# Performance work log

Measured on AMD Instinct MI355X. Metric: run time of the kernel, lower is better.

## Reference

```python
import jax, jax.numpy as jnp
import numpy as np

N, D, K, H = 16384, 2048, 8, 8
HD = D // H
LN_EPS = 1e-5


def setup_inputs() -> dict:
    key = jax.random.key(0)
    ks = jax.random.split(key, 12)
    w = lambda k: jax.random.normal(k, (D, D), dtype=jnp.float32) * 0.02
    return {
        "hidden": jax.random.normal(ks[0], (N, D), dtype=jnp.float32),
        "memory": jax.random.normal(ks[1], (K, D), dtype=jnp.float32) * 0.02,
        "w_read_q": w(ks[2]), "w_read_k": w(ks[3]), "w_read_v": w(ks[4]),
        "w_read_out": w(ks[5]),
        "w_write_q": w(ks[6]), "w_write_k": w(ks[7]), "w_write_v": w(ks[8]),
        "ln_gamma": jnp.ones((D,), dtype=jnp.float32),
        "ln_beta": jnp.zeros((D,), dtype=jnp.float32),
        "gate": jnp.full((1,), -3.0, dtype=jnp.float32),
        "write_gate": jnp.full((1,), -2.0, dtype=jnp.float32),
    }


def _layernorm(x, gamma, beta):
    mu = jnp.mean(x, axis=-1, keepdims=True)
    var = jnp.mean(jnp.square(x - mu), axis=-1, keepdims=True)
    return (x - mu) * jax.lax.rsqrt(var + LN_EPS) * gamma + beta


def reference(hidden, memory, w_read_q, w_read_k, w_read_v, w_read_out,
              w_write_q, w_write_k, w_write_v, ln_gamma, ln_beta, gate, write_gate):
    # --- read: cross-attention from tokens (queries) to memory slots (keys/values) ---
    q = (hidden @ w_read_q.T).reshape(N, H, HD)   # [N,H,hd]
    k = (memory @ w_read_k.T).reshape(K, H, HD)   # [K,H,hd]
    v = (memory @ w_read_v.T).reshape(K, H, HD)
    scores = jnp.einsum("nhd,khd->hnk", q, k) / np.sqrt(HD).astype(np.float32)
    attn = jax.nn.softmax(scores, axis=-1)        # [H,N,K]
    read_out = jnp.einsum("hnk,khd->nhd", attn, v).reshape(N, D)
    cross_info = _layernorm(read_out, ln_gamma, ln_beta) @ w_read_out.T
    g = jax.nn.sigmoid(gate[0])
    result = hidden + g * cross_info              # [N,D]
    # --- write: memory slots (queries) attend over all tokens, gated EMA update ---
    wq = memory @ w_write_q.T                     # [K,D]
    wk = hidden @ w_write_k.T                     # [N,D]
    wv = hidden @ w_write_v.T                     # [N,D]
    wattn = jax.nn.softmax(wq @ wk.T / np.sqrt(D).astype(np.float32), axis=-1)  # [K,N]
    new_info = wattn @ wv                         # [K,D]
    wg = jax.nn.sigmoid(write_gate[0])
    new_memory = (1.0 - wg) * memory + wg * new_info
    return result, new_memory
```

## Files before the change

kernel.cpp:

```cpp
#include <hip/hip_runtime.h>
#include <hip/hip_bf16.h>
#include <stdint.h>

static constexpr int N_ = 16384;
static constexpr int D_ = 2048;
static constexpr float SCALE_R = 1.0f / 16.0f;
static constexpr float SCALE_W = 0.02209708691207961f;

typedef __bf16 bf16x8 __attribute__((ext_vector_type(8)));
typedef float f32x4 __attribute__((ext_vector_type(4)));

__device__ __forceinline__ unsigned short f2bf(float f) {
  unsigned int u = __float_as_uint(f);
  unsigned int r = (u + 0x7fff + ((u >> 16) & 1)) >> 16;
  return (unsigned short)r;
}

__device__ __forceinline__ void lds_load16(void* lds, const void* g) {
  __builtin_amdgcn_global_load_lds(
      (const __attribute__((address_space(1))) uint32_t*)(uintptr_t)g,
      (__attribute__((address_space(3))) uint32_t*)(uint32_t)(uintptr_t)lds,
      16, 0, 0);
}

__global__ __launch_bounds__(256) void k_kvwq(
    const float* __restrict__ mem, const float* __restrict__ wrk,
    const float* __restrict__ wrv, const float* __restrict__ wwq,
    float* __restrict__ kbuf, float* __restrict__ vbuf, float* __restrict__ wqbuf) {
  int gw = (blockIdx.x * 256 + threadIdx.x) >> 6;
  int lane = threadIdx.x & 63;
  int which = gw >> 11;
  int j = gw & 2047;
  const float* W = which == 0 ? wrk : (which == 1 ? wrv : wwq);
  float* O = which == 0 ? kbuf : (which == 1 ? vbuf : wqbuf);
  const f32x4* Wrow = (const f32x4*)(W + (size_t)j * D_);
  const f32x4* M4 = (const f32x4*)mem;
  float acc[8];
#pragma unroll
  for (int kk = 0; kk < 8; ++kk) acc[kk] = 0.f;
#pragma unroll
  for (int t = 0; t < 8; ++t) {
    f32x4 w4 = Wrow[lane + 64 * t];
#pragma unroll
    for (int kk = 0; kk < 8; ++kk) {
      f32x4 m4 = M4[kk * 512 + lane + 64 * t];
      acc[kk] += w4[0] * m4[0] + w4[1] * m4[1] + w4[2] * m4[2] + w4[3] * m4[3];
    }
  }
#pragma unroll
  for (int off = 1; off < 64; off <<= 1)
#pragma unroll
    for (int kk = 0; kk < 8; ++kk) acc[kk] += __shfl_xor(acc[kk], off, 64);
  if (lane == 0) {
#pragma unroll
    for (int kk = 0; kk < 8; ++kk) O[kk * D_ + j] = acc[kk];
  }
}

__global__ __launch_bounds__(256) void k_pr(
    const float* __restrict__ wrq, const float* __restrict__ wwk,
    const float* __restrict__ kbuf, const float* __restrict__ wqbuf,
    float* __restrict__ PRT) {
  int b = blockIdx.x;
  int tid = threadIdx.x;
  bool isP = b < 256;
  int bb = isP ? b : b - 256;
  int q = bb & 3;
  int sub = (bb >> 2) & 7;
  int ic = bb >> 5;
  int i = ic * 256 + tid;
  const float* W = isP ? wrq : wwk;
  const float* V = isP ? kbuf : wqbuf;
  float scale = isP ? SCALE_R : SCALE_W;
  int rowbase = isP ? sub * 8 : 64;
  float acc[8];
#pragma unroll
  for (int kk = 0; kk < 8; ++kk) acc[kk] = 0.f;
  int j0 = sub * 256 + q * 64;
#pragma unroll 4
  for (int jj = 0; jj < 64; ++jj) {
    int j = j0 + jj;
    float wv = W[(size_t)j * D_ + i];
#pragma unroll
    for (int kk = 0; kk < 8; ++kk) acc[kk] += wv * V[kk * D_ + j];
  }
#pragma unroll
  for (int kk = 0; kk < 8; ++kk)
    atomicAdd(&PRT[(rowbase + kk) * D_ + i], acc[kk] * scale);
}

__global__ __launch_bounds__(256) void k_prtb(const float* __restrict__ PRT,
                                              unsigned short* __restrict__ PRTb) {
  int i = (blockIdx.x * 256 + threadIdx.x) * 4;
  f32x4 v = *(const f32x4*)(PRT + i);
  ushort4 o = {f2bf(v[0]), f2bf(v[1]), f2bf(v[2]), f2bf(v[3])};
  *(ushort4*)(PRTb + i) = o;
}

__global__ __launch_bounds__(256) void k_prep(const float* __restrict__ wro,
                                              const float* __restrict__ gamma,
                                              const float* __restrict__ beta,
                                              unsigned short* __restrict__ wp,
                                              float* __restrict__ c1, float* __restrict__ c2) {
  __shared__ float red1[4], red2[4];
  int j = blockIdx.x;
  int tid = threadIdx.x;
  int d = tid * 8;
  const float* src = wro + (size_t)j * D_ + d;
  f32x4 a = *(const f32x4*)src, b = *(const f32x4*)(src + 4);
  f32x4 g0 = *(const f32x4*)(gamma + d), g1 = *(const f32x4*)(gamma + d + 4);
  f32x4 b0 = *(const f32x4*)(beta + d), b1 = *(const f32x4*)(beta + d + 4);
  ushort4 o0, o1;
  o0.x = f2bf(a[0] * g0[0]); o0.y = f2bf(a[1] * g0[1]);
  o0.z = f2bf(a[2] * g0[2]); o0.w = f2bf(a[3] * g0[3]);
  o1.x = f2bf(b[0] * g1[0]); o1.y = f2bf(b[1] * g1[1]);
  o1.z = f2bf(b[2] * g1[2]); o1.w = f2bf(b[3] * g1[3]);
  unsigned short* dst = wp + (size_t)j * D_ + d;
  *(ushort4*)dst = o0;
  *(ushort4*)(dst + 4) = o1;
  float s1 = a[0] * g0[0] + a[1] * g0[1] + a[2] * g0[2] + a[3] * g0[3] +
             b[0] * g1[0] + b[1] * g1[1] + b[2] * g1[2] + b[3] * g1[3];
  float s2 = a[0] * b0[0] + a[1] * b0[1] + a[2] * b0[2] + a[3] * b0[3] +
             b[0] * b1[0] + b[1] * b1[1] + b[2] * b1[2] + b[3] * b1[3];
#pragma unroll
  for (int off = 1; off < 64; off <<= 1) {
    s1 += __shfl_xor(s1, off, 64);
    s2 += __shfl_xor(s2, off, 64);
  }
  int wave = tid >> 6, lane = tid & 63;
  if (lane == 0) { red1[wave] = s1; red2[wave] = s2; }
  __syncthreads();
  if (tid == 0) {
    c1[j] = red1[0] + red1[1] + red1[2] + red1[3];
    c2[j] = red2[0] + red2[1] + red2[2] + red2[3];
  }
}

__global__ __launch_bounds__(256) void k_main(
    const float* __restrict__ hidden, const unsigned short* __restrict__ PRTb,
    const float* __restrict__ vbuf,
    unsigned short* __restrict__ Xhat, float* __restrict__ mu_out,
    float* __restrict__ rstd_out,
    float* __restrict__ upart, float* __restrict__ Zpart) {
  __shared__ unsigned short Ah[2][64 * 64];
  __shared__ unsigned short Bh[2][80 * 64];
  __shared__ unsigned short attnL[64 * 64];
  __shared__ float e8lds[64][8];
  const int tid = threadIdx.x;
  const int row0 = blockIdx.x * 64;
  const int wave = tid >> 6, lane = tid & 63;
  const int fl = lane & 15, fk = lane >> 4;
  const int ar = tid >> 2, acg = tid & 3;

  f32x4 sA0[4], sA1[4];

  auto loadA = [&](f32x4* a, int t) {
    const float* srcA = hidden + (size_t)(row0 + ar) * D_ + t * 64 + acg * 16;
#pragma unroll
    for (int q = 0; q < 4; ++q) a[q] = *(const f32x4*)(srcA + q * 4);
  };
  auto writeA = [&](int buf, f32x4* a) {
#pragma unroll
    for (int hh = 0; hh < 2; ++hh) {
      f32x4 x = a[hh * 2], y = a[hh * 2 + 1];
      ushort4 o0 = {f2bf(x[0]), f2bf(x[1]), f2bf(x[2]), f2bf(x[3])};
      ushort4 o1 = {f2bf(y[0]), f2bf(y[1]), f2bf(y[2]), f2bf(y[3])};
      int idx = (ar * 64 + acg * 16 + hh * 8) ^ ((ar & 7) << 3);
      *(ushort4*)&Ah[buf][idx] = o0;
      *(ushort4*)&Ah[buf][idx + 4] = o1;
    }
  };
  auto stageB = [&](int buf, int kt) {
#pragma unroll
    for (int s = 0; s < 2; ++s) {
      int e = s * 256 + tid;
      int rB = e >> 3, gl = e & 7, gs = gl ^ (rB & 7);
      lds_load16(&Bh[buf][rB * 64 + gl * 8],
                 PRTb + (size_t)rB * D_ + kt * 64 + gs * 8);
    }
    if (tid < 128) {
      int e = 512 + tid;
      int rB = e >> 3, gl = e & 7, gs = gl ^ (rB & 7);
      lds_load16(&Bh[buf][rB * 64 + gl * 8],
                 PRTb + (size_t)rB * D_ + kt * 64 + gs * 8);
    }
  };

  f32x4 acc[5];
#pragma unroll
  for (int n = 0; n < 5; ++n) acc[n] = (f32x4){0.f, 0.f, 0.f, 0.f};

  auto compute = [&](int buf) {
#pragma unroll
    for (int kk = 0; kk < 2; ++kk) {
      int klo = kk * 32 + fk * 8;
      bf16x8 af = *(const bf16x8*)&Ah[buf][((wave * 16 + fl) * 64 + klo) ^ ((fl & 7) << 3)];
#pragma unroll
      for (int n = 0; n < 5; ++n) {
        bf16x8 bf = *(const bf16x8*)&Bh[buf][((n * 16 + fl) * 64 + klo) ^ ((fl & 7) << 3)];
        acc[n] = __builtin_amdgcn_mfma_f32_16x16x32_bf16(af, bf, acc[n], 0, 0, 0);
      }
    }
  };

  loadA(sA0, 0);
  loadA(sA1, 1);
  stageB(0, 0);
  for (int t = 0; t < 32; t += 2) {
    writeA(0, sA0);
    if (t + 2 < 32) loadA(sA0, t + 2);
    __syncthreads();
    stageB(1, t + 1);
    compute(0);
    writeA(1, sA1);
    if (t + 3 < 32) loadA(sA1, t + 3);
    __syncthreads();
    if (t + 2 < 32) stageB(0, t + 2);
    compute(1);
  }

#pragma unroll
  for (int r = 0; r < 4; ++r) {
    int rowl = wave * 16 + fk * 4 + r;
#pragma unroll
    for (int n = 0; n < 4; ++n) {
      float sv = acc[n][r];
      float m = sv;
      m = fmaxf(m, __shfl_xor(m, 1, 64));
      m = fmaxf(m, __shfl_xor(m, 2, 64));
      m = fmaxf(m, __shfl_xor(m, 4, 64));
      float e = __expf(sv - m);
      float ssum = e;
      ssum += __shfl_xor(ssum, 1, 64);
      ssum += __shfl_xor(ssum, 2, 64);
      ssum += __shfl_xor(ssum, 4, 64);
      attnL[rowl * 64 + n * 16 + fl] = f2bf(e / ssum);
    }
    if (fl < 8) e8lds[rowl][fl] = __expf(acc[4][r]);
  }
  __syncthreads();

  float ssum[16], ssq[16];
#pragma unroll
  for (int rw = 0; rw < 16; ++rw) { ssum[rw] = 0.f; ssq[rw] = 0.f; }
#pragma unroll
  for (int c = 0; c < 8; ++c) {
    int d0 = c * 256 + lane * 4;
    f32x4 vv[8];
#pragma unroll
    for (int kk = 0; kk < 8; ++kk) vv[kk] = *(const f32x4*)(vbuf + kk * D_ + d0);
#pragma unroll
    for (int rw = 0; rw < 16; ++rw) {
      bf16x8 at = *(const bf16x8*)&attnL[(wave * 16 + rw) * 64 + c * 8];
      f32x4 ro = (float)at[0] * vv[0] + (float)at[1] * vv[1] +
                 (float)at[2] * vv[2] + (float)at[3] * vv[3] +
                 (float)at[4] * vv[4] + (float)at[5] * vv[5] +
                 (float)at[6] * vv[6] + (float)at[7] * vv[7];
      ssum[rw] += ro[0] + ro[1] + ro[2] + ro[3];
      ssq[rw] += ro[0] * ro[0] + ro[1] * ro[1] + ro[2] * ro[2] + ro[3] * ro[3];
      ushort4 o = {f2bf(ro[0]), f2bf(ro[1]), f2bf(ro[2]), f2bf(ro[3])};
      *(ushort4*)(Xhat + (size_t)(row0 + wave * 16 + rw) * D_ + d0) = o;
    }
  }
  float muv = 0.f, rstdv = 0.f;
#pragma unroll
  for (int rw = 0; rw < 16; ++rw) {
    float s = ssum[rw], q = ssq[rw];
#pragma unroll
    for (int off = 1; off < 64; off <<= 1) {
      s += __shfl_xor(s, off, 64);
      q += __shfl_xor(q, off, 64);
    }
    float m = s * (1.f / 2048.f);
    float var = q * (1.f / 2048.f) - m * m;
    float rs = rsqrtf(var + 1e-5f);
    if (lane == rw) { muv = m; rstdv = rs; }
  }
  if (lane < 16) {
    mu_out[row0 + wave * 16 + lane] = muv;
    rstd_out[row0 + wave * 16 + lane] = rstdv;
  }
  __syncthreads();

  for (int dt = 0; dt < 2; ++dt) {
    int d0 = wave * 512 + dt * 256 + lane * 4;
    f32x4 ua[8];
#pragma unroll
    for (int kk = 0; kk < 8; ++kk) ua[kk] = (f32x4){0.f, 0.f, 0.f, 0.f};
    for (int r8 = 0; r8 < 64; r8 += 8) {
      f32x4 hv[8];
#pragma unroll
      for (int q = 0; q < 8; ++q)
        hv[q] = *(const f32x4*)(hidden + (size_t)(row0 + r8 + q) * D_ + d0);
#pragma unroll
      for (int q = 0; q < 8; ++q) {
        f32x4 e0 = *(const f32x4*)&e8lds[r8 + q][0];
        f32x4 e1 = *(const f32x4*)&e8lds[r8 + q][4];
        ua[0] += e0[0] * hv[q]; ua[1] += e0[1] * hv[q];
        ua[2] += e0[2] * hv[q]; ua[3] += e0[3] * hv[q];
        ua[4] += e1[0] * hv[q]; ua[5] += e1[1] * hv[q];
        ua[6] += e1[2] * hv[q]; ua[7] += e1[3] * hv[q];
      }
    }
#pragma unroll
    for (int kk = 0; kk < 8; ++kk)
      *(f32x4*)(upart + ((size_t)blockIdx.x * 8 + kk) * D_ + d0) = ua[kk];
  }
  if (tid < 8) {
    float z = 0.f;
    for (int r = 0; r < 64; ++r) z += e8lds[r][tid];
    Zpart[blockIdx.x * 8 + tid] = z;
  }
}

__global__ __launch_bounds__(256) void k_ured(const float* __restrict__ upart,
                                              const float* __restrict__ Zpart,
                                              float* __restrict__ tbuf) {
  __shared__ float us[256], zs[256];
  int tid = threadIdx.x;
  int q = tid >> 6;
  int o = blockIdx.x * 64 + (tid & 63);
  int kk = o >> 11, d = o & 2047;
  float z = 0.f, u = 0.f;
#pragma unroll 4
  for (int b = q * 64; b < q * 64 + 64; ++b) {
    z += Zpart[b * 8 + kk];
    u += upart[((size_t)b * 8 + kk) * 2048 + d];
  }
  us[tid] = u; zs[tid] = z;
  __syncthreads();
  if (q == 0) {
    u += us[tid + 64] + us[tid + 128] + us[tid + 192];
    z += zs[tid + 64] + zs[tid + 128] + zs[tid + 192];
    tbuf[o] = u / z;
  }
}

__global__ __launch_bounds__(256) void k_newmem(
    const float* __restrict__ tbuf, const float* __restrict__ wwv,
    const float* __restrict__ mem, const float* __restrict__ wgate,
    float* __restrict__ out_mem) {
  int j = (blockIdx.x * 256 + threadIdx.x) >> 6;
  int lane = threadIdx.x & 63;
  const f32x4* Wrow = (const f32x4*)(wwv + (size_t)j * D_);
  const f32x4* T4 = (const f32x4*)tbuf;
  float acc[8];
#pragma unroll
  for (int kk = 0; kk < 8; ++kk) acc[kk] = 0.f;
#pragma unroll
  for (int t = 0; t < 8; ++t) {
    f32x4 w4 = Wrow[lane + 64 * t];
#pragma unroll
    for (int kk = 0; kk < 8; ++kk) {
      f32x4 t4 = T4[kk * 512 + lane + 64 * t];
      acc[kk] += w4[0] * t4[0] + w4[1] * t4[1] + w4[2] * t4[2] + w4[3] * t4[3];
    }
  }
#pragma unroll
  for (int off = 1; off < 64; off <<= 1)
#pragma unroll
    for (int kk = 0; kk < 8; ++kk) acc[kk] += __shfl_xor(acc[kk], off, 64);
  if (lane == 0) {
    float wg = 1.f / (1.f + __expf(-wgate[0]));
#pragma unroll
    for (int kk = 0; kk < 8; ++kk)
      out_mem[kk * D_ + j] = (1.f - wg) * mem[kk * D_ + j] + wg * acc[kk];
  }
}

__global__ __launch_bounds__(256) void k_gemm(
    const unsigned short* __restrict__ A,
    const unsigned short* __restrict__ B,
    const float* __restrict__ hidden, const float* __restrict__ gate,
    const float* __restrict__ mu, const float* __restrict__ rstd,
    const float* __restrict__ c1, const float* __restrict__ c2,
    float* __restrict__ out) {
  __shared__ unsigned short As[2][128 * 64];
  __shared__ unsigned short Bs[2][128 * 64];
  const int tid = threadIdx.x;
  const int bm = blockIdx.x >> 4, bn = blockIdx.x & 15;
  const int row0 = bm * 128, col0 = bn * 128;
  const int wave = tid >> 6, lane = tid & 63;
  const int wr = wave >> 1, wc = wave & 1;
  const int fl = lane & 15, fk = lane >> 4;
  const int srow = tid >> 3;
  const int scol_l = (tid & 7) * 8;
  const int scol_g = ((tid & 7) ^ (srow & 7)) * 8;

  f32x4 acc[4][4];
#pragma unroll
  for (int m = 0; m < 4; ++m)
#pragma unroll
    for (int n = 0; n < 4; ++n) acc[m][n] = (f32x4){0.f, 0.f, 0.f, 0.f};

  auto stage = [&](int buf, int kt) {
    const int k0 = kt * 64;
#pragma unroll
    for (int p = 0; p < 4; ++p) {
      int r = srow + p * 32;
      lds_load16(&As[buf][r * 64 + scol_l], A + (size_t)(row0 + r) * D_ + k0 + scol_g);
      lds_load16(&Bs[buf][r * 64 + scol_l], B + (size_t)(col0 + r) * D_ + k0 + scol_g);
    }
  };

  stage(0, 0);
  for (int kt = 0; kt < 32; ++kt) {
    __syncthreads();
    if (kt + 1 < 32) stage((kt + 1) & 1, kt + 1);
    const int cb = kt & 1;
#pragma unroll
    for (int kkk = 0; kkk < 2; ++kkk) {
      const int gsw = ((kkk * 4 + fk) ^ (fl & 7)) * 8;
      bf16x8 af[4], bfr[4];
#pragma unroll
      for (int m = 0; m < 4; ++m)
        af[m] = *(const bf16x8*)&As[cb][(wr * 64 + m * 16 + fl) * 64 + gsw];
#pragma unroll
      for (int n = 0; n < 4; ++n)
        bfr[n] = *(const bf16x8*)&Bs[cb][(wc * 64 + n * 16 + fl) * 64 + gsw];
#pragma unroll
      for (int m = 0; m < 4; ++m)
#pragma unroll
        for (int n = 0; n < 4; ++n)
          acc[m][n] = __builtin_amdgcn_mfma_f32_16x16x32_bf16(af[m], bfr[n], acc[m][n], 0, 0, 0);
    }
  }
  float g = 1.f / (1.f + __expf(-gate[0]));
  int cols[4];
  float C1v[4], C2v[4];
#pragma unroll
  for (int n = 0; n < 4; ++n) {
    cols[n] = col0 + wc * 64 + n * 16 + fl;
    C1v[n] = c1[cols[n]] * g;
    C2v[n] = c2[cols[n]] * g;
  }
#pragma unroll
  for (int m = 0; m < 4; ++m)
#pragma unroll
    for (int r = 0; r < 4; ++r) {
      int row = row0 + wr * 64 + m * 16 + fk * 4 + r;
      float RS = rstd[row], MU = mu[row];
      const float* hrow = hidden + (size_t)row * D_;
      float* orow = out + (size_t)row * D_;
#pragma unroll
      for (int n = 0; n < 4; ++n)
        orow[cols[n]] = hrow[cols[n]] + g * RS * acc[m][n][r] - RS * MU * C1v[n] + C2v[n];
    }
}

extern "C" void kernel_launch(void* const* d_in, const int* in_sizes, int n_in,
                              void* d_out, int out_size, void* d_ws, size_t ws_size,
                              hipStream_t stream) {
  const float* hidden = (const float*)d_in[0];
  const float* mem    = (const float*)d_in[1];
  const float* wrq = (const float*)d_in[2];
  const float* wrk = (const float*)d_in[3];
  const float* wrv = (const float*)d_in[4];
  const float* wro = (const float*)d_in[5];
  const float* wwq = (const float*)d_in[6];
  const float* wwk = (const float*)d_in[7];
  const float* wwv = (const float*)d_in[8];
  const float* gamma = (const float*)d_in[9];
  const float* beta  = (const float*)d_in[10];
  const float* gate  = (const float*)d_in[11];
  const float* wgate = (const float*)d_in[12];
  float* out = (float*)d_out;

  char* ws = (char*)d_ws;
  float* kbuf  = (float*)(ws);
  float* vbuf  = (float*)(ws + (64 << 10));
  float* wqbuf = (float*)(ws + (128 << 10));
  float* PRT   = (float*)(ws + (192 << 10));
  float* tbuf  = (float*)(ws + (832 << 10));
  float* Zpart = (float*)(ws + (896 << 10));
  float* c1    = (float*)(ws + (904 << 10));
  float* c2    = (float*)(ws + (912 << 10));
  unsigned short* PRTb = (unsigned short*)(ws + (960 << 10));
  float* upart = (float*)(ws + (1536ull << 10));
  unsigned short* Wp   = (unsigned short*)(ws + (1536ull << 10) + (16ull << 20));
  unsigned short* Xhat = (unsigned short*)(ws + (1536ull << 10) + (24ull << 20));
  float* mu   = kbuf;
  float* rstd = wqbuf;

  hipMemsetAsync(PRT, 0, 80 * 2048 * sizeof(float), stream);
  k_prep<<<2048, 256, 0, stream>>>(wro, gamma, beta, Wp, c1, c2);
  k_kvwq<<<1536, 256, 0, stream>>>(mem, wrk, wrv, wwq, kbuf, vbuf, wqbuf);
  k_pr<<<512, 256, 0, stream>>>(wrq, wwk, kbuf, wqbuf, PRT);
  k_prtb<<<160, 256, 0, stream>>>(PRT, PRTb);
  k_main<<<256, 256, 0, stream>>>(hidden, PRTb, vbuf, Xhat, mu, rstd, upart, Zpart);
  k_ured<<<256, 256, 0, stream>>>(upart, Zpart, tbuf);
  k_newmem<<<512, 256, 0, stream>>>(tbuf, wwv, mem, wgate, out + (size_t)N_ * D_);
  k_gemm<<<2048, 256, 0, stream>>>(Xhat, Wp, hidden, gate, mu, rstd, c1, c2, out);
}
```

Measured before the change: 333.7 us.

## Merge independent small kernels into combined launches and split k_pr finer

Three independent front kernels (weight prep, memory projections, PRT memset) become one launch, with blocks dispatched by index. The new-memory GEMV is likewise folded into the big output GEMM launch as extra blocks. k_pr's reduction chunk is halved to 32 rows, doubling its block count for more parallelism at the cost of twice as many atomic adds. The aim is to cut launch overhead and let small independent work overlap, at the cost of heavier block-divergent kernels that may raise register and LDS pressure.

```diff
diff --git a/kernel.cpp b/kernel.cpp
--- a/kernel.cpp
+++ b/kernel.cpp
@@ -23,37 +23,80 @@
       16, 0, 0);
 }
 
-__global__ __launch_bounds__(256) void k_kvwq(
+__global__ __launch_bounds__(256) void k_front(
+    const float* __restrict__ wro, const float* __restrict__ gamma,
+    const float* __restrict__ beta, unsigned short* __restrict__ wp,
+    float* __restrict__ c1, float* __restrict__ c2,
     const float* __restrict__ mem, const float* __restrict__ wrk,
     const float* __restrict__ wrv, const float* __restrict__ wwq,
-    float* __restrict__ kbuf, float* __restrict__ vbuf, float* __restrict__ wqbuf) {
-  int gw = (blockIdx.x * 256 + threadIdx.x) >> 6;
-  int lane = threadIdx.x & 63;
-  int which = gw >> 11;
-  int j = gw & 2047;
-  const float* W = which == 0 ? wrk : (which == 1 ? wrv : wwq);
-  float* O = which == 0 ? kbuf : (which == 1 ? vbuf : wqbuf);
-  const f32x4* Wrow = (const f32x4*)(W + (size_t)j * D_);
-  const f32x4* M4 = (const f32x4*)mem;
-  float acc[8];
-#pragma unroll
-  for (int kk = 0; kk < 8; ++kk) acc[kk] = 0.f;
-#pragma unroll
-  for (int t = 0; t < 8; ++t) {
-    f32x4 w4 = Wrow[lane + 64 * t];
-#pragma unroll
-    for (int kk = 0; kk < 8; ++kk) {
-      f32x4 m4 = M4[kk * 512 + lane + 64 * t];
-      acc[kk] += w4[0] * m4[0] + w4[1] * m4[1] + w4[2] * m4[2] + w4[3] * m4[3];
-    }
-  }
-#pragma unroll
-  for (int off = 1; off < 64; off <<= 1)
-#pragma unroll
-    for (int kk = 0; kk < 8; ++kk) acc[kk] += __shfl_xor(acc[kk], off, 64);
-  if (lane == 0) {
-#pragma unroll
-    for (int kk = 0; kk < 8; ++kk) O[kk * D_ + j] = acc[kk];
+    float* __restrict__ kbuf, float* __restrict__ vbuf,
+    float* __restrict__ wqbuf, float* __restrict__ PRT) {
+  __shared__ float red1[4], red2[4];
+  const int b = blockIdx.x;
+  const int tid = threadIdx.x;
+  if (b < 2048) {
+    int j = b;
+    int d = tid * 8;
+    const float* src = wro + (size_t)j * D_ + d;
+    f32x4 a = *(const f32x4*)src, bb = *(const f32x4*)(src + 4);
+    f32x4 g0 = *(const f32x4*)(gamma + d), g1 = *(const f32x4*)(gamma + d + 4);
+    f32x4 b0 = *(const f32x4*)(beta + d), b1 = *(const f32x4*)(beta + d + 4);
+    ushort4 o0, o1;
+    o0.x = f2bf(a[0] * g0[0]); o0.y = f2bf(a[1] * g0[1]);
+    o0.z = f2bf(a[2] * g0[2]); o0.w = f2bf(a[3] * g0[3]);
+    o1.x = f2bf(bb[0] * g1[0]); o1.y = f2bf(bb[1] * g1[1]);
+    o1.z = f2bf(bb[2] * g1[2]); o1.w = f2bf(bb[3] * g1[3]);
+    unsigned short* dst = wp + (size_t)j * D_ + d;
+    *(ushort4*)dst = o0;
+    *(ushort4*)(dst + 4) = o1;
+    float s1 = a[0] * g0[0] + a[1] * g0[1] + a[2] * g0[2] + a[3] * g0[3] +
+               bb[0] * g1[0] + bb[1] * g1[1] + bb[2] * g1[2] + bb[3] * g1[3];
+    float s2 = a[0] * b0[0] + a[1] * b0[1] + a[2] * b0[2] + a[3] * b0[3] +
+               bb[0] * b1[0] + bb[1] * b1[1] + bb[2] * b1[2] + bb[3] * b1[3];
+#pragma unroll
+    for (int off = 1; off < 64; off <<= 1) {
+      s1 += __shfl_xor(s1, off, 64);
+      s2 += __shfl_xor(s2, off, 64);
+    }
+    int wave = tid >> 6, lane = tid & 63;
+    if (lane == 0) { red1[wave] = s1; red2[wave] = s2; }
+    __syncthreads();
+    if (tid == 0) {
+      c1[j] = red1[0] + red1[1] + red1[2] + red1[3];
+      c2[j] = red2[0] + red2[1] + red2[2] + red2[3];
+    }
+  } else if (b < 3584) {
+    int gw = ((b - 2048) * 256 + tid) >> 6;
+    int lane = tid & 63;
+    int which = gw >> 11;
+    int j = gw & 2047;
+    const float* W = which == 0 ? wrk : (which == 1 ? wrv : wwq);
+    float* O = which == 0 ? kbuf : (which == 1 ? vbuf : wqbuf);
+    const f32x4* Wrow = (const f32x4*)(W + (size_t)j * D_);
+    const f32x4* M4 = (const f32x4*)mem;
+    float acc[8];
+#pragma unroll
+    for (int kk = 0; kk < 8; ++kk) acc[kk] = 0.f;
+#pragma unroll
+    for (int t = 0; t < 8; ++t) {
+      f32x4 w4 = Wrow[lane + 64 * t];
+#pragma unroll
+      for (int kk = 0; kk < 8; ++kk) {
+        f32x4 m4 = M4[kk * 512 + lane + 64 * t];
+        acc[kk] += w4[0] * m4[0] + w4[1] * m4[1] + w4[2] * m4[2] + w4[3] * m4[3];
+      }
+    }
+#pragma unroll
+    for (int off = 1; off < 64; off <<= 1)
+#pragma unroll
+      for (int kk = 0; kk < 8; ++kk) acc[kk] += __shfl_xor(acc[kk], off, 64);
+    if (lane == 0) {
+#pragma unroll
+      for (int kk = 0; kk < 8; ++kk) O[kk * D_ + j] = acc[kk];
+    }
+  } else {
+    int idx = (b - 3584) * 256 + tid;
+    ((f32x4*)PRT)[idx] = (f32x4){0.f, 0.f, 0.f, 0.f};
   }
 }
 
@@ -63,11 +106,11 @@
     float* __restrict__ PRT) {
   int b = blockIdx.x;
   int tid = threadIdx.x;
-  bool isP = b < 256;
-  int bb = isP ? b : b - 256;
-  int q = bb & 3;
-  int sub = (bb >> 2) & 7;
-  int ic = bb >> 5;
+  bool isP = b < 512;
+  int bb = isP ? b : b - 512;
+  int oct = bb & 7;
+  int sub = (bb >> 3) & 7;
+  int ic = bb >> 6;
   int i = ic * 256 + tid;
   const float* W = isP ? wrq : wwk;
   const float* V = isP ? kbuf : wqbuf;
@@ -76,9 +119,9 @@
   float acc[8];
 #pragma unroll
   for (int kk = 0; kk < 8; ++kk) acc[kk] = 0.f;
-  int j0 = sub * 256 + q * 64;
+  int j0 = sub * 256 + oct * 32;
 #pragma unroll 4
-  for (int jj = 0; jj < 64; ++jj) {
+  for (int jj = 0; jj < 32; ++jj) {
     int j = j0 + jj;
     float wv = W[(size_t)j * D_ + i];
 #pragma unroll
@@ -95,45 +138,6 @@
   f32x4 v = *(const f32x4*)(PRT + i);
   ushort4 o = {f2bf(v[0]), f2bf(v[1]), f2bf(v[2]), f2bf(v[3])};
   *(ushort4*)(PRTb + i) = o;
-}
-
-__global__ __launch_bounds__(256) void k_prep(const float* __restrict__ wro,
-                                              const float* __restrict__ gamma,
-                                              const float* __restrict__ beta,
-                                              unsigned short* __restrict__ wp,
-                                              float* __restrict__ c1, float* __restrict__ c2) {
-  __shared__ float red1[4], red2[4];
-  int j = blockIdx.x;
-  int tid = threadIdx.x;
-  int d = tid * 8;
-  const float* src = wro + (size_t)j * D_ + d;
-  f32x4 a = *(const f32x4*)src, b = *(const f32x4*)(src + 4);
-  f32x4 g0 = *(const f32x4*)(gamma + d), g1 = *(const f32x4*)(gamma + d + 4);
-  f32x4 b0 = *(const f32x4*)(beta + d), b1 = *(const f32x4*)(beta + d + 4);
-  ushort4 o0, o1;
-  o0.x = f2bf(a[0] * g0[0]); o0.y = f2bf(a[1] * g0[1]);
-  o0.z = f2bf(a[2] * g0[2]); o0.w = f2bf(a[3] * g0[3]);
-  o1.x = f2bf(b[0] * g1[0]); o1.y = f2bf(b[1] * g1[1]);
-  o1.z = f2bf(b[2] * g1[2]); o1.w = f2bf(b[3] * g1[3]);
-  unsigned short* dst = wp + (size_t)j * D_ + d;
-  *(ushort4*)dst = o0;
-  *(ushort4*)(dst + 4) = o1;
-  float s1 = a[0] * g0[0] + a[1] * g0[1] + a[2] * g0[2] + a[3] * g0[3] +
-             b[0] * g1[0] + b[1] * g1[1] + b[2] * g1[2] + b[3] * g1[3];
-  float s2 = a[0] * b0[0] + a[1] * b0[1] + a[2] * b0[2] + a[3] * b0[3] +
-             b[0] * b1[0] + b[1] * b1[1] + b[2] * b1[2] + b[3] * b1[3];
-#pragma unroll
-  for (int off = 1; off < 64; off <<= 1) {
-    s1 += __shfl_xor(s1, off, 64);
-    s2 += __shfl_xor(s2, off, 64);
-  }
-  int wave = tid >> 6, lane = tid & 63;
-  if (lane == 0) { red1[wave] = s1; red2[wave] = s2; }
-  __syncthreads();
-  if (tid == 0) {
-    c1[j] = red1[0] + red1[1] + red1[2] + red1[3];
-    c2[j] = red2[0] + red2[1] + red2[2] + red2[3];
-  }
 }
 
 __global__ __launch_bounds__(256) void k_main(
@@ -336,48 +340,49 @@
   }
 }
 
-__global__ __launch_bounds__(256) void k_newmem(
-    const float* __restrict__ tbuf, const float* __restrict__ wwv,
-    const float* __restrict__ mem, const float* __restrict__ wgate,
-    float* __restrict__ out_mem) {
-  int j = (blockIdx.x * 256 + threadIdx.x) >> 6;
-  int lane = threadIdx.x & 63;
-  const f32x4* Wrow = (const f32x4*)(wwv + (size_t)j * D_);
-  const f32x4* T4 = (const f32x4*)tbuf;
-  float acc[8];
-#pragma unroll
-  for (int kk = 0; kk < 8; ++kk) acc[kk] = 0.f;
-#pragma unroll
-  for (int t = 0; t < 8; ++t) {
-    f32x4 w4 = Wrow[lane + 64 * t];
-#pragma unroll
-    for (int kk = 0; kk < 8; ++kk) {
-      f32x4 t4 = T4[kk * 512 + lane + 64 * t];
-      acc[kk] += w4[0] * t4[0] + w4[1] * t4[1] + w4[2] * t4[2] + w4[3] * t4[3];
-    }
-  }
-#pragma unroll
-  for (int off = 1; off < 64; off <<= 1)
-#pragma unroll
-    for (int kk = 0; kk < 8; ++kk) acc[kk] += __shfl_xor(acc[kk], off, 64);
-  if (lane == 0) {
-    float wg = 1.f / (1.f + __expf(-wgate[0]));
-#pragma unroll
-    for (int kk = 0; kk < 8; ++kk)
-      out_mem[kk * D_ + j] = (1.f - wg) * mem[kk * D_ + j] + wg * acc[kk];
-  }
-}
-
-__global__ __launch_bounds__(256) void k_gemm(
+__global__ __launch_bounds__(256) void k_big(
     const unsigned short* __restrict__ A,
     const unsigned short* __restrict__ B,
     const float* __restrict__ hidden, const float* __restrict__ gate,
     const float* __restrict__ mu, const float* __restrict__ rstd,
     const float* __restrict__ c1, const float* __restrict__ c2,
-    float* __restrict__ out) {
+    float* __restrict__ out,
+    const float* __restrict__ tbuf, const float* __restrict__ wwv,
+    const float* __restrict__ mem, const float* __restrict__ wgate,
+    float* __restrict__ out_mem) {
   __shared__ unsigned short As[2][128 * 64];
   __shared__ unsigned short Bs[2][128 * 64];
   const int tid = threadIdx.x;
+  if (blockIdx.x >= 2048) {
+    int vb = blockIdx.x - 2048;
+    int j = (vb * 256 + tid) >> 6;
+    int lane = tid & 63;
+    const f32x4* Wrow = (const f32x4*)(wwv + (size_t)j * D_);
+    const f32x4* T4 = (const f32x4*)tbuf;
+    float acc[8];
+#pragma unroll
+    for (int kk = 0; kk < 8; ++kk) acc[kk] = 0.f;
+#pragma unroll
+    for (int t = 0; t < 8; ++t) {
+      f32x4 w4 = Wrow[lane + 64 * t];
+#pragma unroll
+      for (int kk = 0; kk < 8; ++kk) {
+        f32x4 t4 = T4[kk * 512 + lane + 64 * t];
+        acc[kk] += w4[0] * t4[0] + w4[1] * t4[1] + w4[2] * t4[2] + w4[3] * t4[3];
+      }
+    }
+#pragma unroll
+    for (int off = 1; off < 64; off <<= 1)
+#pragma unroll
+      for (int kk = 0; kk < 8; ++kk) acc[kk] += __shfl_xor(acc[kk], off, 64);
+    if (lane == 0) {
+      float wg = 1.f / (1.f + __expf(-wgate[0]));
+#pragma unroll
+      for (int kk = 0; kk < 8; ++kk)
+        out_mem[kk * D_ + j] = (1.f - wg) * mem[kk * D_ + j] + wg * acc[kk];
+    }
+    return;
+  }
   const int bm = blockIdx.x >> 4, bn = blockIdx.x & 15;
   const int row0 = bm * 128, col0 = bn * 128;
   const int wave = tid >> 6, lane = tid & 63;
@@ -482,13 +487,12 @@
   float* mu   = kbuf;
   float* rstd = wqbuf;
 
-  hipMemsetAsync(PRT, 0, 80 * 2048 * sizeof(float), stream);
-  k_prep<<<2048, 256, 0, stream>>>(wro, gamma, beta, Wp, c1, c2);
-  k_kvwq<<<1536, 256, 0, stream>>>(mem, wrk, wrv, wwq, kbuf, vbuf, wqbuf);
-  k_pr<<<512, 256, 0, stream>>>(wrq, wwk, kbuf, wqbuf, PRT);
+  k_front<<<3744, 256, 0, stream>>>(wro, gamma, beta, Wp, c1, c2,
+                                    mem, wrk, wrv, wwq, kbuf, vbuf, wqbuf, PRT);
+  k_pr<<<1024, 256, 0, stream>>>(wrq, wwk, kbuf, wqbuf, PRT);
   k_prtb<<<160, 256, 0, stream>>>(PRT, PRTb);
   k_main<<<256, 256, 0, stream>>>(hidden, PRTb, vbuf, Xhat, mu, rstd, upart, Zpart);
   k_ured<<<256, 256, 0, stream>>>(upart, Zpart, tbuf);
-  k_newmem<<<512, 256, 0, stream>>>(tbuf, wwv, mem, wgate, out + (size_t)N_ * D_);
-  k_gemm<<<2048, 256, 0, stream>>>(Xhat, Wp, hidden, gate, mu, rstd, c1, c2, out);
-}
+  k_big<<<2560, 256, 0, stream>>>(Xhat, Wp, hidden, gate, mu, rstd, c1, c2, out,
+                                  tbuf, wwv, mem, wgate, out + (size_t)N_ * D_);
+}
```

Measured after the change: 322.8 us. -3.3%, faster.
